# Optimization experiments

Hardware: AMD Instinct MI355X
Metric: run time of the kernel (lower is better)

## Reference

```python
import jax, jax.numpy as jnp
import numpy as np

B, T, C, H = 4, 2048, 1024, 16
HS = C // H  # head_size = 64
EPS = 1e-5


def setup_inputs() -> dict:
    key = jax.random.key(0)
    ks = jax.random.split(key, 16)
    s = 0.02
    inp = {
        "x": jax.random.normal(ks[0], (B, T, C), jnp.float32),
        # custom LayerNorm buffers (gamma=ones, beta=zeros in source)
        "ln1_g": jnp.ones((C,), jnp.float32),
        "ln1_b": jnp.zeros((C,), jnp.float32),
        "ln2_g": jnp.ones((C,), jnp.float32),
        "ln2_b": jnp.zeros((C,), jnp.float32),
        # per-head Q/K/V linears, stacked over heads: [H, C, HS]
        "Wq": jax.random.normal(ks[1], (H, C, HS), jnp.float32) * s,
        "bq": jax.random.normal(ks[2], (H, HS), jnp.float32) * s,
        "Wk": jax.random.normal(ks[3], (H, C, HS), jnp.float32) * s,
        "bk": jax.random.normal(ks[4], (H, HS), jnp.float32) * s,
        "Wv": jax.random.normal(ks[5], (H, C, HS), jnp.float32) * s,
        "bv": jax.random.normal(ks[6], (H, HS), jnp.float32) * s,
        # output projection [C, C]
        "Wo": jax.random.normal(ks[7], (C, C), jnp.float32) * s,
        "bo": jax.random.normal(ks[8], (C,), jnp.float32) * s,
        # FFN: C -> 4C -> C
        "W1": jax.random.normal(ks[9], (C, 4 * C), jnp.float32) * s,
        "b1": jax.random.normal(ks[10], (4 * C,), jnp.float32) * s,
        "W2": jax.random.normal(ks[11], (4 * C, C), jnp.float32) * s,
        "b2": jax.random.normal(ks[12], (C,), jnp.float32) * s,
    }
    return inp


def _layernorm_time_axis(x, g, b):
    # Faithful to source: normalizes over axis=1 (time), unbiased variance (ddof=1).
    m = jnp.mean(x, axis=1, keepdims=True)
    v = jnp.var(x, axis=1, keepdims=True, ddof=1)
    return g * (x - m) / jnp.sqrt(v + EPS) + b


def reference(x, ln1_g, ln1_b, ln2_g, ln2_b, Wq, bq, Wk, bk, Wv, bv, Wo, bo, W1, b1, W2, b2):
    Bc, Tc, Cc = x.shape
    h = _layernorm_time_axis(x, ln1_g, ln1_b)
    # per-head projections: [B, H, T, HS]
    q = jnp.einsum('btc,hcd->bhtd', h, Wq) + bq[None, :, None, :]
    k = jnp.einsum('btc,hcd->bhtd', h, Wk) + bk[None, :, None, :]
    v = jnp.einsum('btc,hcd->bhtd', h, Wv) + bv[None, :, None, :]
    # scores scaled by C**-0.5 (full embed dim, as in source)
    wei = jnp.einsum('bhtd,bhsd->bhts', q, k) * (Cc ** -0.5)
    causal = jnp.tril(jnp.ones((Tc, Tc), bool))
    wei = jnp.where(causal[None, None], wei, -jnp.inf)
    wei = jax.nn.softmax(wei, axis=-1)
    att = jnp.einsum('bhts,bhsd->bhtd', wei, v)
    # concat heads -> [B, T, C], then projection
    att = att.transpose(0, 2, 1, 3).reshape(Bc, Tc, Cc)
    x = x + att @ Wo + bo
    # FFN on ln2
    h2 = _layernorm_time_axis(x, ln2_g, ln2_b)
    ff = jax.nn.relu(h2 @ W1 + b1) @ W2 + b2
    return x + ff
```

## Files before the change

### kernel.cpp

```cpp
#include <hip/hip_runtime.h>

#define B_   4
#define T_   2048
#define C_   1024
#define H_   16
#define HS_  64
#define BT_  (B_*T_)
#define EPS_ 1e-5f

typedef unsigned short u16;
typedef unsigned int   u32;
typedef __attribute__((ext_vector_type(8))) __bf16 bf16x8;
typedef __attribute__((ext_vector_type(4))) float  f32x4;
typedef __attribute__((ext_vector_type(8))) u16    u16x8;
typedef __attribute__((ext_vector_type(4))) u16    u16x4;
typedef __attribute__((ext_vector_type(4))) u32    u32x4;

__device__ __forceinline__ u16 f2bf(float f) {
  unsigned x = __builtin_bit_cast(unsigned, f);
  x += 0x7fffu + ((x >> 16) & 1u);
  return (u16)(x >> 16);
}
__device__ __forceinline__ float bf2f(u16 v) {
  return __builtin_bit_cast(float, (u32)v << 16);
}

__device__ __forceinline__ float fast_exp2(float x) {
  float y;
  asm("v_exp_f32 %0, %1" : "=v"(y) : "v"(x));
  return y;
}
__device__ __forceinline__ float fast_rcp(float x) {
  float y;
  asm("v_rcp_f32 %0, %1" : "=v"(y) : "v"(x));
  return y;
}

#define GLD_LDS16(src, dst) \
  __builtin_amdgcn_global_load_lds((__attribute__((address_space(1))) void*)(src), \
                                   (__attribute__((address_space(3))) void*)(dst), 16, 0, 0)

__global__ __launch_bounds__(256) void ln_partial(const float* __restrict__ x,
                                                  float* __restrict__ ps,
                                                  float* __restrict__ psq) {
  int col = blockIdx.x * 256 + threadIdx.x;
  int b = col >> 10, c = col & (C_ - 1);
  int t0 = blockIdx.y * (T_ / 16);
  const float* p = x + (size_t)b * T_ * C_ + (size_t)t0 * C_ + c;
  float s = 0.f, sq = 0.f;
  #pragma unroll 4
  for (int i = 0; i < T_ / 16; ++i) { float v = p[(size_t)i * C_]; s += v; sq += v * v; }
  ps [blockIdx.y * (B_ * C_) + col] = s;
  psq[blockIdx.y * (B_ * C_) + col] = sq;
}

__global__ __launch_bounds__(256) void ln_partial_bf(const u16* __restrict__ x,
                                                     float* __restrict__ ps,
                                                     float* __restrict__ psq) {
  int col = blockIdx.x * 256 + threadIdx.x;
  int b = col >> 10, c = col & (C_ - 1);
  int t0 = blockIdx.y * (T_ / 16);
  const u16* p = x + (size_t)b * T_ * C_ + (size_t)t0 * C_ + c;
  float s = 0.f, sq = 0.f;
  #pragma unroll 4
  for (int i = 0; i < T_ / 16; ++i) { float v = bf2f(p[(size_t)i * C_]); s += v; sq += v * v; }
  ps [blockIdx.y * (B_ * C_) + col] = s;
  psq[blockIdx.y * (B_ * C_) + col] = sq;
}

__global__ __launch_bounds__(256) void ln_final(const float* __restrict__ ps,
                                                const float* __restrict__ psq,
                                                float* __restrict__ mean,
                                                float* __restrict__ rstd) {
  int col = blockIdx.x * 256 + threadIdx.x;
  float s = 0.f, sq = 0.f;
  #pragma unroll
  for (int i = 0; i < 16; ++i) { s += ps[i * (B_ * C_) + col]; sq += psq[i * (B_ * C_) + col]; }
  float m = s * (1.f / T_);
  float var = (sq - (float)T_ * m * m) * (1.f / (T_ - 1));
  mean[col] = m;
  rstd[col] = rsqrtf(var + EPS_);
}

__global__ __launch_bounds__(256) void ln_norm(const float* __restrict__ x,
                                               const float* __restrict__ mean,
                                               const float* __restrict__ rstd,
                                               const float* __restrict__ gam,
                                               const float* __restrict__ bet,
                                               u16* __restrict__ out) {
  size_t i = ((size_t)blockIdx.x * 256 + threadIdx.x) * 4;
  int c  = (int)(i & (C_ - 1));
  int b  = (int)(i >> 21);
  int bc = (b << 10) + c;
  float4 v = *(const float4*)(x + i);
  float vv[4] = {v.x, v.y, v.z, v.w};
  u16x4 o;
  #pragma unroll
  for (int j = 0; j < 4; ++j)
    o[j] = f2bf(gam[c + j] * (vv[j] - mean[bc + j]) * rstd[bc + j] + bet[c + j]);
  *(u16x4*)(out + i) = o;
}

__global__ __launch_bounds__(256) void ln_norm_bf(const u16* __restrict__ x,
                                                  const float* __restrict__ mean,
                                                  const float* __restrict__ rstd,
                                                  const float* __restrict__ gam,
                                                  const float* __restrict__ bet,
                                                  u16* __restrict__ out) {
  size_t i = ((size_t)blockIdx.x * 256 + threadIdx.x) * 4;
  int c  = (int)(i & (C_ - 1));
  int b  = (int)(i >> 21);
  int bc = (b << 10) + c;
  u16x4 v = *(const u16x4*)(x + i);
  u16x4 o;
  #pragma unroll
  for (int j = 0; j < 4; ++j)
    o[j] = f2bf(gam[c + j] * (bf2f(v[j]) - mean[bc + j]) * rstd[bc + j] + bet[c + j]);
  *(u16x4*)(out + i) = o;
}

__global__ __launch_bounds__(256) void transpose_cast(const float* __restrict__ in,
                                                      u16* __restrict__ out,
                                                      int cols_in, int ld_out,
                                                      size_t batch_in, size_t batch_out) {
  __shared__ float tile[32][33];
  const float* I = in + (size_t)blockIdx.z * batch_in;
  u16* Ou = out + (size_t)blockIdx.z * batch_out;
  int r0 = blockIdx.y << 5, c0 = blockIdx.x << 5;
  int tx = threadIdx.x & 31, ty = threadIdx.x >> 5;
  #pragma unroll
  for (int rr = 0; rr < 32; rr += 8)
    tile[ty + rr][tx] = I[(size_t)(r0 + ty + rr) * cols_in + c0 + tx];
  __syncthreads();
  #pragma unroll
  for (int rr = 0; rr < 32; rr += 8)
    Ou[(size_t)(c0 + ty + rr) * ld_out + r0 + tx] = f2bf(tile[tx][ty + rr]);
}

__global__ __launch_bounds__(256) void concat_bias(const float* __restrict__ bq,
                                                   const float* __restrict__ bk,
                                                   const float* __restrict__ bv,
                                                   float* __restrict__ out) {
  int i = blockIdx.x * 256 + threadIdx.x;
  float v = (i < 1024) ? bq[i] : (i < 2048 ? bk[i - 1024] : bv[i - 2048]);
  out[i] = v;
}

__global__ __launch_bounds__(256) void v_transpose(const u16* __restrict__ qkv,
                                                   u16* __restrict__ Vt) {
  __shared__ u16 tile[32][33];
  int bh = blockIdx.z; int b = bh >> 4, h = bh & 15;
  int t0 = blockIdx.x << 5, hs0 = blockIdx.y << 5;
  int tx = threadIdx.x & 31, ty = threadIdx.x >> 5;
  const u16* src = qkv + (size_t)(b * T_ + t0) * 3072 + 2048 + h * 64 + hs0;
  #pragma unroll
  for (int rr = 0; rr < 32; rr += 8)
    tile[ty + rr][tx] = src[(size_t)(ty + rr) * 3072 + tx];
  __syncthreads();
  u16* dst = Vt + ((size_t)bh * 64 + hs0) * T_ + t0;
  #pragma unroll
  for (int rr = 0; rr < 32; rr += 8)
    dst[(size_t)(ty + rr) * T_ + tx] = tile[tx][ty + rr];
}

template<int BN, int RELU, int QSCALE>
__global__ __launch_bounds__(256, 2)
void gemm_128t(const u16* __restrict__ A,
               const u16* __restrict__ Bt,
               const float* __restrict__ bias,
               u16* __restrict__ outp,
               int M, int N, int K) {
  constexpr int BK  = 32;
  constexpr int CHA = 2;
  constexpr int CHB = BN / 64;
  constexpr int NF  = BN / 32;

  __shared__ u16 sA[3][128 * BK];
  __shared__ u16 sB[3][BN * BK];

  const int tid = threadIdx.x;
  const int wave = tid >> 6, lane = tid & 63;
  const int g = lane >> 4, r16 = lane & 15;

  const int nbx = N / BN;
  const int nwg = gridDim.x;
  const int bid = blockIdx.x;
  const int swz = ((bid & 7) * (nwg >> 3)) + (bid >> 3);
  const int bx = swz % nbx, by = swz / nbx;
  const int row0 = by << 7, col0 = bx * BN;

  const u16* aS[CHA];
  const u16* bS[CHB];
  #pragma unroll
  for (int j = 0; j < CHA; ++j) {
    const int ci = tid + 256 * j, row = ci >> 2, cc = ci & 3;
    aS[j] = A + (size_t)(row0 + row) * K + ((cc ^ ((row >> 1) & 3)) * 8);
  }
  #pragma unroll
  for (int j = 0; j < CHB; ++j) {
    const int ci = tid + 256 * j, row = ci >> 2, cc = ci & 3;
    bS[j] = Bt + (size_t)(col0 + row) * K + ((cc ^ ((row >> 1) & 3)) * 8);
  }
  const int ldsOff = wave * 512;

  auto stage = [&](int t, int buf) {
    const int ko = t * BK;
    #pragma unroll
    for (int j = 0; j < CHA; ++j)
      GLD_LDS16(aS[j] + ko, &sA[buf][ldsOff + j * 2048]);
    #pragma unroll
    for (int j = 0; j < CHB; ++j)
      GLD_LDS16(bS[j] + ko, &sB[buf][ldsOff + j * 2048]);
  };

  auto wait_stage1 = [&]() {
    if constexpr (CHB == 4) asm volatile("s_waitcnt vmcnt(6)" ::: "memory");
    else                    asm volatile("s_waitcnt vmcnt(5)" ::: "memory");
  };

  const int wrow = (wave >> 1) * 64;
  const int wcol = (wave & 1) * (BN >> 1);
  f32x4 acc[4][NF] = {};

  const int NT = K / BK;

  stage(0, 0); stage(1, 1);
  wait_stage1();
  __builtin_amdgcn_s_barrier();
  __builtin_amdgcn_sched_barrier(0);

  for (int t = 0; t < NT; ++t) {
    const u16* As = sA[t % 3];
    const u16* Bs = sB[t % 3];
    bf16x8 af[4], bf[NF];
    #pragma unroll
    for (int m = 0; m < 4; ++m) {
      const int lr = wrow + m * 16 + r16;
      af[m] = *(const bf16x8*)&As[lr * 32 + ((g ^ ((lr >> 1) & 3)) * 8)];
    }
    #pragma unroll
    for (int n = 0; n < NF; ++n) {
      const int lr = wcol + n * 16 + r16;
      bf[n] = *(const bf16x8*)&Bs[lr * 32 + ((g ^ ((lr >> 1) & 3)) * 8)];
    }
    if (t + 2 < NT) stage(t + 2, (t + 2) % 3);

    __builtin_amdgcn_s_setprio(1);
    #pragma unroll
    for (int m = 0; m < 4; ++m)
      #pragma unroll
      for (int n = 0; n < NF; ++n)
        acc[m][n] = __builtin_amdgcn_mfma_f32_16x16x32_bf16(af[m], bf[n], acc[m][n], 0, 0, 0);
    __builtin_amdgcn_s_setprio(0);

    if (t + 1 < NT) {
      if (t + 2 < NT) wait_stage1();
      else            asm volatile("s_waitcnt vmcnt(0)" ::: "memory");
      __builtin_amdgcn_s_barrier();
      __builtin_amdgcn_sched_barrier(0);
    }
  }

  #pragma unroll
  for (int m = 0; m < 4; ++m) {
    #pragma unroll
    for (int n = 0; n < NF; ++n) {
      const int col = col0 + wcol + n * 16 + r16;
      const float bv = bias[col];
      const float sc = (QSCALE && col < 1024) ? 0.04508422003f : 1.f;
      const int rowb = row0 + wrow + m * 16 + g * 4;
      #pragma unroll
      for (int r = 0; r < 4; ++r) {
        float v = acc[m][n][r] + bv;
        if (RELU) v = fmaxf(v, 0.f);
        if (QSCALE) v *= sc;
        outp[(size_t)(rowb + r) * N + col] = f2bf(v);
      }
    }
  }
}

template<int RELU, int RAW, int QSCALE>
__global__ __launch_bounds__(512, 2)
void gemm_256(const u16* __restrict__ A,
              const u16* __restrict__ Bt,
              const float* __restrict__ bias,
              const u16* __restrict__ resb,
              void* __restrict__ outp,
              void* __restrict__ outp_b,
              int M, int N, int K) {
  constexpr int BK = 32;
  __shared__ u16 sA[4][256 * BK];
  __shared__ u16 sB[4][256 * BK];

  const int tid = threadIdx.x;
  const int wave = tid >> 6, lane = tid & 63;
  const int g = lane >> 4, r16 = lane & 15;

  const int nbx = N >> 8;
  const int nwg = gridDim.x;
  const int bid = blockIdx.x;
  const int swz = ((bid & 7) * (nwg >> 3)) + (bid >> 3);
  const int bx = swz % nbx, by = swz / nbx;
  const int row0 = by << 8, col0 = bx << 8;

  const int kspan = RAW ? (K >> 1) : K;
  const int kbase = RAW ? ((int)blockIdx.y * kspan) : 0;

  const u16* aS[2];
  const u16* bS[2];
  #pragma unroll
  for (int j = 0; j < 2; ++j) {
    const int ci = tid + 512 * j, row = ci >> 2, cc = ci & 3;
    aS[j] = A  + (size_t)(row0 + row) * K + ((cc ^ ((row >> 1) & 3)) * 8) + kbase;
    bS[j] = Bt + (size_t)(col0 + row) * K + ((cc ^ ((row >> 1) & 3)) * 8) + kbase;
  }
  const int ldsOff = wave * 512;

  auto stage = [&](int t, int buf) {
    const int ko = t * BK;
    #pragma unroll
    for (int j = 0; j < 2; ++j)
      GLD_LDS16(aS[j] + ko, &sA[buf][ldsOff + j * 4096]);
    #pragma unroll
    for (int j = 0; j < 2; ++j)
      GLD_LDS16(bS[j] + ko, &sB[buf][ldsOff + j * 4096]);
  };

  const int wrow = (wave >> 2) * 128;
  const int wcol = (wave & 3) * 64;
  f32x4 acc[8][4] = {};

  const int NT = kspan / BK;

  stage(0, 0); stage(1, 1);
  asm volatile("s_waitcnt vmcnt(4)" ::: "memory");
  __builtin_amdgcn_s_barrier();
  __builtin_amdgcn_sched_barrier(0);

  for (int t = 0; t < NT; ++t) {
    const u16* As = sA[t & 3];
    const u16* Bs = sB[t & 3];
    bf16x8 af[8], bf[4];
    #pragma unroll
    for (int m = 0; m < 8; ++m) {
      const int lr = wrow + m * 16 + r16;
      af[m] = *(const bf16x8*)&As[lr * 32 + ((g ^ ((lr >> 1) & 3)) * 8)];
    }
    #pragma unroll
    for (int n = 0; n < 4; ++n) {
      const int lr = wcol + n * 16 + r16;
      bf[n] = *(const bf16x8*)&Bs[lr * 32 + ((g ^ ((lr >> 1) & 3)) * 8)];
    }
    if (t + 2 < NT) stage(t + 2, (t + 2) & 3);

    __builtin_amdgcn_s_setprio(1);
    #pragma unroll
    for (int m = 0; m < 8; ++m)
      #pragma unroll
      for (int n = 0; n < 4; ++n)
        acc[m][n] = __builtin_amdgcn_mfma_f32_16x16x32_bf16(af[m], bf[n], acc[m][n], 0, 0, 0);
    __builtin_amdgcn_s_setprio(0);

    if (t + 1 < NT) {
      if (t + 2 < NT) asm volatile("s_waitcnt vmcnt(4)" ::: "memory");
      else            asm volatile("s_waitcnt vmcnt(0)" ::: "memory");
      __builtin_amdgcn_s_barrier();
      __builtin_amdgcn_sched_barrier(0);
    }
  }

  if constexpr (RAW) {
    if (blockIdx.y) {
      float* po = (float*)outp_b;
      #pragma unroll
      for (int m = 0; m < 8; ++m) {
        #pragma unroll
        for (int n = 0; n < 4; ++n) {
          const int col = col0 + wcol + n * 16 + r16;
          const float bv = bias[col];
          const int rowb = row0 + wrow + m * 16 + g * 4;
          #pragma unroll
          for (int r = 0; r < 4; ++r) {
            const size_t idx = (size_t)(rowb + r) * N + col;
            po[idx] = acc[m][n][r] + bv + bf2f(resb[idx]);
          }
        }
      }
    } else {
      float* po = (float*)outp;
      #pragma unroll
      for (int m = 0; m < 8; ++m) {
        #pragma unroll
        for (int n = 0; n < 4; ++n) {
          const int col = col0 + wcol + n * 16 + r16;
          const int rowb = row0 + wrow + m * 16 + g * 4;
          #pragma unroll
          for (int r = 0; r < 4; ++r)
            po[(size_t)(rowb + r) * N + col] = acc[m][n][r];
        }
      }
    }
  } else {
    u16* po = (u16*)outp;
    #pragma unroll
    for (int m = 0; m < 8; ++m) {
      #pragma unroll
      for (int n = 0; n < 4; ++n) {
        const int col = col0 + wcol + n * 16 + r16;
        const float bv = bias[col];
        const float sc = (QSCALE && col < 1024) ? 0.04508422003f : 1.f;
        const int rowb = row0 + wrow + m * 16 + g * 4;
        #pragma unroll
        for (int r = 0; r < 4; ++r) {
          float v = acc[m][n][r] + bv;
          if (RELU) v = fmaxf(v, 0.f);
          if (QSCALE) v *= sc;
          po[(size_t)(rowb + r) * N + col] = f2bf(v);
        }
      }
    }
  }
}

__global__ __launch_bounds__(256) void ffn2_reduce(const float* __restrict__ pA,
                                                   float* __restrict__ out) {
  size_t i = ((size_t)blockIdx.x * 256 + threadIdx.x) * 4;
  float4 a = *(const float4*)(pA + i);
  float4 o = *(const float4*)(out + i);
  float4 v;
  v.x = a.x + o.x;
  v.y = a.y + o.y;
  v.z = a.z + o.z;
  v.w = a.w + o.w;
  *(float4*)(out + i) = v;
}

template<int BM, int BN, int THREADS, int OUT_F32, int RELU, int RES>
__global__ __launch_bounds__(THREADS, 3)
void gemm_pipe(const u16* __restrict__ A,
               const u16* __restrict__ Bt,
               const float* __restrict__ bias,
               const float* __restrict__ res,
               void* __restrict__ outp,
               int M, int N, int K) {
  constexpr int BK  = 32;
  constexpr int CHA = (BM * 4) / THREADS;
  constexpr int CHB = (BN * 4) / THREADS;
  constexpr int CH  = CHA + CHB;

  __shared__ u16 sA[3][BM * BK];
  __shared__ u16 sB[3][BN * BK];

  const int tid = threadIdx.x;
  const int wave = tid >> 6, lane = tid & 63;
  const int g = lane >> 4, r16 = lane & 15;

  const int nbx = N / BN;
  const int nwg = gridDim.x;
  const int bid = blockIdx.x;
  const int swz = ((bid & 7) * (nwg >> 3)) + (bid >> 3);
  const int bx = swz % nbx, by = swz / nbx;
  const int row0 = by * BM, col0 = bx * BN;

  const u16* aS[CHA];
  const u16* bS[CHB];
  #pragma unroll
  for (int j = 0; j < CHA; ++j) {
    const int ci = tid + THREADS * j, row = ci >> 2, cc = ci & 3;
    aS[j] = A + (size_t)(row0 + row) * K + ((cc ^ ((row >> 1) & 3)) * 8);
  }
  #pragma unroll
  for (int j = 0; j < CHB; ++j) {
    const int ci = tid + THREADS * j, row = ci >> 2, cc = ci & 3;
    bS[j] = Bt + (size_t)(col0 + row) * K + ((cc ^ ((row >> 1) & 3)) * 8);
  }
  const int ldsOff = wave * 512;

  auto stage = [&](int t, int buf) {
    const int ko = t * BK;
    #pragma unroll
    for (int j = 0; j < CHA; ++j)
      GLD_LDS16(aS[j] + ko, &sA[buf][ldsOff + j * (THREADS * 8)]);
    #pragma unroll
    for (int j = 0; j < CHB; ++j)
      GLD_LDS16(bS[j] + ko, &sB[buf][ldsOff + j * (THREADS * 8)]);
  };

  const int wrow = (wave >> 1) * 64;
  const int wcol = (wave & 1) * 64;
  f32x4 acc[4][4] = {};

  const int NT = K / BK;

  stage(0, 0); stage(1, 1);
  if constexpr (CH == 3) asm volatile("s_waitcnt vmcnt(3)" ::: "memory");
  else                   asm volatile("s_waitcnt vmcnt(4)" ::: "memory");
  __builtin_amdgcn_s_barrier();
  __builtin_amdgcn_sched_barrier(0);

  for (int t = 0; t < NT; ++t) {
    if (t + 2 < NT) stage(t + 2, (t + 2) % 3);
    const u16* As = sA[t % 3];
    const u16* Bs = sB[t % 3];
    bf16x8 af[4], bf[4];
    #pragma unroll
    for (int m = 0; m < 4; ++m) {
      const int lr = wrow + m * 16 + r16;
      af[m] = *(const bf16x8*)&As[lr * 32 + ((g ^ ((lr >> 1) & 3)) * 8)];
    }
    #pragma unroll
    for (int n = 0; n < 4; ++n) {
      const int lr = wcol + n * 16 + r16;
      bf[n] = *(const bf16x8*)&Bs[lr * 32 + ((g ^ ((lr >> 1) & 3)) * 8)];
    }
    __builtin_amdgcn_s_setprio(1);
    #pragma unroll
    for (int m = 0; m < 4; ++m)
      #pragma unroll
      for (int n = 0; n < 4; ++n)
        acc[m][n] = __builtin_amdgcn_mfma_f32_16x16x32_bf16(af[m], bf[n], acc[m][n], 0, 0, 0);
    __builtin_amdgcn_s_setprio(0);

    if (t + 1 < NT) {
      if (t + 2 < NT) {
        if constexpr (CH == 3) asm volatile("s_waitcnt vmcnt(3)" ::: "memory");
        else                   asm volatile("s_waitcnt vmcnt(4)" ::: "memory");
      } else {
        asm volatile("s_waitcnt vmcnt(0)" ::: "memory");
      }
      __builtin_amdgcn_s_barrier();
      __builtin_amdgcn_sched_barrier(0);
    }
  }

  #pragma unroll
  for (int m = 0; m < 4; ++m) {
    #pragma unroll
    for (int n = 0; n < 4; ++n) {
      const int col = col0 + wcol + n * 16 + r16;
      const float bv = bias[col];
      const int rowb = row0 + wrow + m * 16 + g * 4;
      #pragma unroll
      for (int r = 0; r < 4; ++r) {
        const size_t idx = (size_t)(rowb + r) * N + col;
        float v = acc[m][n][r] + bv;
        if (RES)  v += res[idx];
        if (RELU) v = fmaxf(v, 0.f);
        if (OUT_F32) ((float*)outp)[idx] = v;
        else         ((u16*)outp)[idx]   = f2bf(v);
      }
    }
  }
}

__global__ __launch_bounds__(256, 4) void attn_fwd(const u16* __restrict__ qkv,
                                                   const u16* __restrict__ Vt,
                                                   u16* __restrict__ O) {
  __shared__ u16 sK[2][64 * 64];
  __shared__ u16 sV[2][64 * 64];

  const int orig = blockIdx.x;
  const int work = ((orig & 7) << 7) + (orig >> 3);
  const int i = work & 15;
  const int h = (work >> 4) & 15;
  const int b = work >> 8;
  const int qA = i << 6, qB = (31 - i) << 6;
  const int nA = i + 1,  nB = 32 - i;

  const int tid = threadIdx.x, wave = tid >> 6, lane = tid & 63;
  const int g = lane >> 4, r16 = lane & 15;

  const size_t base = (size_t)b * T_ * 3072 + h * 64;
  const u16* Qp = qkv + base;
  const u16* Kp = qkv + base + 1024;
  const u16* VtP = Vt + (size_t)(b * 16 + h) * 64 * T_;

  const int rowL = lane >> 3;
  const int colL = 8 * ((lane & 7) ^ rowL);
  const u16* kSrc = Kp  + (size_t)(wave * 16 + rowL) * 3072 + colL;
  const u16* vSrc = VtP + (size_t)(wave * 16 + rowL) * T_   + colL;
  u16* kDst0 = &sK[0][(wave * 16 + 0) * 64];
  u16* kDst8 = &sK[0][(wave * 16 + 8) * 64];
  u16* vDst0 = &sV[0][(wave * 16 + 0) * 64];
  u16* vDst8 = &sV[0][(wave * 16 + 8) * 64];

  const int ck0 = (( 0 + g * 16) ^ ((r16 & 7) << 4)) >> 1;
  const int ck1 = ((64 + g * 16) ^ ((r16 & 7) << 4)) >> 1;

  bf16x8 qfA[2], qfB[2];
  #pragma unroll
  for (int kc = 0; kc < 2; ++kc) {
    qfA[kc] = *(const bf16x8*)(Qp + (size_t)(qA + wave * 16 + r16) * 3072 + kc * 32 + g * 8);
    qfB[kc] = *(const bf16x8*)(Qp + (size_t)(qB + wave * 16 + r16) * 3072 + kc * 32 + g * 8);
  }

  f32x4 accA[4] = {}, accB[4] = {};
  f32x4 lA4 = {}, lB4 = {};
  const int qaA = qA + wave * 16 + r16;
  const int qaB = qB + wave * 16 + r16;

  const u32 one2 = 0x3F803F80u;
  const u32x4 onesv = {one2, one2, one2, one2};
  const bf16x8 ONES = __builtin_bit_cast(bf16x8, onesv);

  int sbuf = 0;
  auto stageAdv = [&]() {
    const int o = sbuf * 4096;
    GLD_LDS16(kSrc,            kDst0 + o);
    GLD_LDS16(kSrc + 8 * 3072, kDst8 + o);
    GLD_LDS16(vSrc,            vDst0 + o);
    GLD_LDS16(vSrc + 8 * T_,   vDst8 + o);
    kSrc += 64 * 3072;
    vSrc += 64;
    sbuf ^= 1;
  };

  auto qkt = [&](const bf16x8* kf0, const bf16x8* kf1, const bf16x8* qf, f32x4* s) {
    __builtin_amdgcn_s_setprio(1);
    #pragma unroll
    for (int ni = 0; ni < 4; ++ni) {
      f32x4 t = {};
      t = __builtin_amdgcn_mfma_f32_16x16x32_bf16(kf0[ni], qf[0], t, 0, 0, 0);
      t = __builtin_amdgcn_mfma_f32_16x16x32_bf16(kf1[ni], qf[1], t, 0, 0, 0);
      s[ni] = t;
    }
    __builtin_amdgcn_s_setprio(0);
  };

  auto softmax_pack = [&](f32x4* s, bool diag, int q_abs, int kv0, bf16x8* pa) {
    if (diag) {
      #pragma unroll
      for (int ni = 0; ni < 4; ++ni)
        #pragma unroll
        for (int r = 0; r < 4; ++r) {
          const int kv_abs = kv0 + ni * 16 + g * 4 + r;
          if (kv_abs > q_abs) s[ni][r] = -3e38f;
        }
    }
    #pragma unroll
    for (int ni = 0; ni < 4; ++ni)
      #pragma unroll
      for (int r = 0; r < 4; ++r)
        s[ni][r] = fast_exp2(s[ni][r]);

    u32 pk[4][2];
    #pragma unroll
    for (int ni = 0; ni < 4; ++ni)
      #pragma unroll
      for (int h2 = 0; h2 < 2; ++h2)
        asm("v_cvt_pk_bf16_f32 %0, %1, %2"
            : "=v"(pk[ni][h2]) : "v"(s[ni][2 * h2]), "v"(s[ni][2 * h2 + 1]));

    u32 pa32[2][4];
    #pragma unroll
    for (int kc = 0; kc < 2; ++kc)
      #pragma unroll
      for (int h2 = 0; h2 < 2; ++h2) {
        u32 a = pk[2 * kc][h2], bq_ = pk[2 * kc + 1][h2];
        asm("v_permlane32_swap_b32 %0, %1" : "+v"(a), "+v"(bq_));
        asm("v_permlane16_swap_b32 %0, %1" : "+v"(a), "+v"(bq_));
        pa32[kc][h2] = a;
        pa32[kc][2 + h2] = bq_;
      }
    #pragma unroll
    for (int kc = 0; kc < 2; ++kc) {
      u32x4 tmp = {pa32[kc][0], pa32[kc][1], pa32[kc][2], pa32[kc][3]};
      pa[kc] = __builtin_bit_cast(bf16x8, tmp);
    }
  };

  stageAdv();
  asm volatile("s_waitcnt vmcnt(0)" ::: "memory");
  __builtin_amdgcn_s_barrier();
  __builtin_amdgcn_sched_barrier(0);

  int cbuf = 0;
  for (int t = 0; t < nB; ++t) {
    if (t + 1 < nB) stageAdv();
    const u16* Kb = sK[cbuf];
    const u16* Vb = sV[cbuf];
    const int kv0 = t << 6;
    const bool actA = (t < nA);

    bf16x8 kf0[4], kf1[4];
    #pragma unroll
    for (int ni = 0; ni < 4; ++ni) {
      kf0[ni] = *(const bf16x8*)&Kb[(ni * 16 + r16) * 64 + ck0];
      kf1[ni] = *(const bf16x8*)&Kb[(ni * 16 + r16) * 64 + ck1];
    }

    f32x4 s[4];
    bf16x8 paB[2], paA[2];

    qkt(kf0, kf1, qfB, s);
    softmax_pack(s, t == nB - 1, qaB, kv0, paB);
    if (actA) {
      qkt(kf0, kf1, qfA, s);
      softmax_pack(s, t == nA - 1, qaA, kv0, paA);
    }

    bf16x8 vf0[4], vf1[4];
    #pragma unroll
    for (int hsb = 0; hsb < 4; ++hsb) {
      vf0[hsb] = *(const bf16x8*)&Vb[(hsb * 16 + r16) * 64 + ck0];
      vf1[hsb] = *(const bf16x8*)&Vb[(hsb * 16 + r16) * 64 + ck1];
    }

    __builtin_amdgcn_s_setprio(1);
    lB4 = __builtin_amdgcn_mfma_f32_16x16x32_bf16(paB[0], ONES, lB4, 0, 0, 0);
    lB4 = __builtin_amdgcn_mfma_f32_16x16x32_bf16(paB[1], ONES, lB4, 0, 0, 0);
    #pragma unroll
    for (int hsb = 0; hsb < 4; ++hsb) {
      accB[hsb] = __builtin_amdgcn_mfma_f32_16x16x32_bf16(paB[0], vf0[hsb], accB[hsb], 0, 0, 0);
      accB[hsb] = __builtin_amdgcn_mfma_f32_16x16x32_bf16(paB[1], vf1[hsb], accB[hsb], 0, 0, 0);
    }
    if (actA) {
      lA4 = __builtin_amdgcn_mfma_f32_16x16x32_bf16(paA[0], ONES, lA4, 0, 0, 0);
      lA4 = __builtin_amdgcn_mfma_f32_16x16x32_bf16(paA[1], ONES, lA4, 0, 0, 0);
      #pragma unroll
      for (int hsb = 0; hsb < 4; ++hsb) {
        accA[hsb] = __builtin_amdgcn_mfma_f32_16x16x32_bf16(paA[0], vf0[hsb], accA[hsb], 0, 0, 0);
        accA[hsb] = __builtin_amdgcn_mfma_f32_16x16x32_bf16(paA[1], vf1[hsb], accA[hsb], 0, 0, 0);
      }
    }
    __builtin_amdgcn_s_setprio(0);

    if (t + 1 < nB) {
      asm volatile("s_waitcnt vmcnt(0)" ::: "memory");
      __builtin_amdgcn_s_barrier();
      __builtin_amdgcn_sched_barrier(0);
    }
    cbuf ^= 1;
  }

  float rlA[4], rlB[4];
  #pragma unroll
  for (int r = 0; r < 4; ++r) {
    rlA[r] = fast_rcp(lA4[r]);
    rlB[r] = fast_rcp(lB4[r]);
  }
  #pragma unroll
  for (int hsb = 0; hsb < 4; ++hsb)
    #pragma unroll
    for (int r = 0; r < 4; ++r) {
      const size_t rowA = (size_t)b * T_ + qA + wave * 16 + g * 4 + r;
      const size_t rowB = (size_t)b * T_ + qB + wave * 16 + g * 4 + r;
      O[rowA * C_ + h * 64 + hsb * 16 + r16] = f2bf(accA[hsb][r] * rlA[r]);
      O[rowB * C_ + h * 64 + hsb * 16 + r16] = f2bf(accB[hsb][r] * rlB[r]);
    }
}

extern "C" void kernel_launch(void* const* d_in, const int* in_sizes, int n_in,
                              void* d_out, int out_size, void* d_ws, size_t ws_size,
                              hipStream_t stream) {
  const float* x    = (const float*)d_in[0];
  const float* ln1g = (const float*)d_in[1];
  const float* ln1b = (const float*)d_in[2];
  const float* ln2g = (const float*)d_in[3];
  const float* ln2b = (const float*)d_in[4];
  const float* Wq   = (const float*)d_in[5];
  const float* bq   = (const float*)d_in[6];
  const float* Wk   = (const float*)d_in[7];
  const float* bk   = (const float*)d_in[8];
  const float* Wv   = (const float*)d_in[9];
  const float* bv   = (const float*)d_in[10];
  const float* Wo   = (const float*)d_in[11];
  const float* bo   = (const float*)d_in[12];
  const float* W1   = (const float*)d_in[13];
  const float* b1   = (const float*)d_in[14];
  const float* W2   = (const float*)d_in[15];
  const float* b2   = (const float*)d_in[16];

  char* w = (char*)d_ws;
  float* ps    = (float*)(w + 0);
  float* psq   = (float*)(w + 262144);
  float* mean  = (float*)(w + 524288);
  float* rstd  = (float*)(w + 540672);
  float* bqkv  = (float*)(w + 557056);
  u16*   h     = (u16*)  (w + 573440);
  u16*   wqkvT = (u16*)  (w + 17350656);
  u16*   woT   = (u16*)  (w + 23642112);
  u16*   w1T   = (u16*)  (w + 25739264);
  u16*   w2T   = (u16*)  (w + 34127872);
  u16*   x1b   = (u16*)  (w + 42516480);
  u16*   Vt    = (u16*)  (w + 59293696);
  u16*   qkv   = (u16*)  (w + 76070912);
  u16*   Oo    = (u16*)  (w + 126402560);
  u16*   u     = qkv;
  float* pA    = (float*)(w + 573440);

  transpose_cast<<<dim3(2, 32, 16), 256, 0, stream>>>(Wq, wqkvT,                     64,   1024, (size_t)C_ * 64, (size_t)64 * 1024);
  transpose_cast<<<dim3(2, 32, 16), 256, 0, stream>>>(Wk, wqkvT + (size_t)1024*1024, 64,   1024, (size_t)C_ * 64, (size_t)64 * 1024);
  transpose_cast<<<dim3(2, 32, 16), 256, 0, stream>>>(Wv, wqkvT + (size_t)2048*1024, 64,   1024, (size_t)C_ * 64, (size_t)64 * 1024);
  transpose_cast<<<dim3(32, 32, 1), 256, 0, stream>>>(Wo, woT, 1024, 1024, 0, 0);
  transpose_cast<<<dim3(128, 32, 1), 256, 0, stream>>>(W1, w1T, 4096, 1024, 0, 0);
  transpose_cast<<<dim3(32, 128, 1), 256, 0, stream>>>(W2, w2T, 1024, 4096, 0, 0);
  concat_bias<<<12, 256, 0, stream>>>(bq, bk, bv, bqkv);

  ln_partial<<<dim3(16, 16), 256, 0, stream>>>(x, ps, psq);
  ln_final<<<16, 256, 0, stream>>>(ps, psq, mean, rstd);
  ln_norm<<<8192, 256, 0, stream>>>(x, mean, rstd, ln1g, ln1b, h);

  gemm_128t<192, 0, 1><<<1024, 256, 0, stream>>>(h, wqkvT, bqkv, qkv, BT_, 3072, 1024);

  v_transpose<<<dim3(T_ / 32, 2, B_ * H_), 256, 0, stream>>>(qkv, Vt);

  attn_fwd<<<1024, 256, 0, stream>>>(qkv, Vt, Oo);

  gemm_pipe<128, 128, 256, 0, 0, 1><<<512, 256, 0, stream>>>(Oo, woT, bo, x, x1b, BT_, 1024, 1024);

  ln_partial_bf<<<dim3(16, 16), 256, 0, stream>>>(x1b, ps, psq);
  ln_final<<<16, 256, 0, stream>>>(ps, psq, mean, rstd);
  ln_norm_bf<<<8192, 256, 0, stream>>>(x1b, mean, rstd, ln2g, ln2b, h);

  gemm_128t<256, 1, 0><<<1024, 256, 0, stream>>>(h, w1T, b1, u, BT_, 4096, 1024);
  gemm_256<0, 1, 0><<<dim3(128, 2), 512, 0, stream>>>(u, w2T, b2, x1b, pA, d_out, BT_, 1024, 4096);
  ffn2_reduce<<<8192, 256, 0, stream>>>(pA, (float*)d_out);
}
```

Baseline: 393.4 us.

## Process 128-row query tiles per attention block to double K/V reuse

```diff
diff --git a/kernel.cpp b/kernel.cpp
--- a/kernel.cpp
+++ b/kernel.cpp
@@ -554,19 +554,19 @@
   }
 }
 
-__global__ __launch_bounds__(256, 4) void attn_fwd(const u16* __restrict__ qkv,
+__global__ __launch_bounds__(256, 2) void attn_fwd(const u16* __restrict__ qkv,
                                                    const u16* __restrict__ Vt,
                                                    u16* __restrict__ O) {
   __shared__ u16 sK[2][64 * 64];
   __shared__ u16 sV[2][64 * 64];
 
   const int orig = blockIdx.x;
-  const int work = ((orig & 7) << 7) + (orig >> 3);
-  const int i = work & 15;
-  const int h = (work >> 4) & 15;
-  const int b = work >> 8;
-  const int qA = i << 6, qB = (31 - i) << 6;
-  const int nA = i + 1,  nB = 32 - i;
+  const int work = ((orig & 7) << 6) + (orig >> 3);
+  const int i = work & 7;
+  const int h = (work >> 3) & 15;
+  const int b = work >> 7;
+  const int qA = i << 7, qB = (15 - i) << 7;
+  const int nA = 2 * i + 2, nB = 32 - 2 * i;
 
   const int tid = threadIdx.x, wave = tid >> 6, lane = tid & 63;
   const int g = lane >> 4, r16 = lane & 15;
@@ -588,17 +588,23 @@
   const int ck0 = (( 0 + g * 16) ^ ((r16 & 7) << 4)) >> 1;
   const int ck1 = ((64 + g * 16) ^ ((r16 & 7) << 4)) >> 1;
 
-  bf16x8 qfA[2], qfB[2];
-  #pragma unroll
-  for (int kc = 0; kc < 2; ++kc) {
-    qfA[kc] = *(const bf16x8*)(Qp + (size_t)(qA + wave * 16 + r16) * 3072 + kc * 32 + g * 8);
-    qfB[kc] = *(const bf16x8*)(Qp + (size_t)(qB + wave * 16 + r16) * 3072 + kc * 32 + g * 8);
-  }
-
-  f32x4 accA[4] = {}, accB[4] = {};
-  f32x4 lA4 = {}, lB4 = {};
-  const int qaA = qA + wave * 16 + r16;
-  const int qaB = qB + wave * 16 + r16;
+  bf16x8 qfA[2][2], qfB[2][2];
+  #pragma unroll
+  for (int qp = 0; qp < 2; ++qp)
+    #pragma unroll
+    for (int kc = 0; kc < 2; ++kc) {
+      qfA[qp][kc] = *(const bf16x8*)(Qp + (size_t)(qA + wave * 32 + qp * 16 + r16) * 3072 + kc * 32 + g * 8);
+      qfB[qp][kc] = *(const bf16x8*)(Qp + (size_t)(qB + wave * 32 + qp * 16 + r16) * 3072 + kc * 32 + g * 8);
+    }
+
+  f32x4 accA[2][4] = {}, accB[2][4] = {};
+  f32x4 lA[2] = {}, lB[2] = {};
+  int qaA[2], qaB[2];
+  #pragma unroll
+  for (int qp = 0; qp < 2; ++qp) {
+    qaA[qp] = qA + wave * 32 + qp * 16 + r16;
+    qaB[qp] = qB + wave * 32 + qp * 16 + r16;
+  }
 
   const u32 one2 = 0x3F803F80u;
   const u32x4 onesv = {one2, one2, one2, one2};
@@ -682,49 +688,53 @@
     const u16* Vb = sV[cbuf];
     const int kv0 = t << 6;
     const bool actA = (t < nA);
-
-    bf16x8 kf0[4], kf1[4];
+    const bool mB = (t + 2 >= nB);
+    const bool mA = (t + 2 >= nA);
+
+    bf16x8 kf0[4], kf1[4], vf0[4], vf1[4];
     #pragma unroll
     for (int ni = 0; ni < 4; ++ni) {
       kf0[ni] = *(const bf16x8*)&Kb[(ni * 16 + r16) * 64 + ck0];
       kf1[ni] = *(const bf16x8*)&Kb[(ni * 16 + r16) * 64 + ck1];
-    }
-
-    f32x4 s[4];
-    bf16x8 paB[2], paA[2];
-
-    qkt(kf0, kf1, qfB, s);
-    softmax_pack(s, t == nB - 1, qaB, kv0, paB);
+      vf0[ni] = *(const bf16x8*)&Vb[(ni * 16 + r16) * 64 + ck0];
+      vf1[ni] = *(const bf16x8*)&Vb[(ni * 16 + r16) * 64 + ck1];
+    }
+
+    #pragma unroll
+    for (int qp = 0; qp < 2; ++qp) {
+      f32x4 s[4];
+      bf16x8 pa[2];
+      qkt(kf0, kf1, qfB[qp], s);
+      softmax_pack(s, mB, qaB[qp], kv0, pa);
+      __builtin_amdgcn_s_setprio(1);
+      lB[qp] = __builtin_amdgcn_mfma_f32_16x16x32_bf16(pa[0], ONES, lB[qp], 0, 0, 0);
+      lB[qp] = __builtin_amdgcn_mfma_f32_16x16x32_bf16(pa[1], ONES, lB[qp], 0, 0, 0);
+      #pragma unroll
+      for (int hsb = 0; hsb < 4; ++hsb) {
+        accB[qp][hsb] = __builtin_amdgcn_mfma_f32_16x16x32_bf16(pa[0], vf0[hsb], accB[qp][hsb], 0, 0, 0);
+        accB[qp][hsb] = __builtin_amdgcn_mfma_f32_16x16x32_bf16(pa[1], vf1[hsb], accB[qp][hsb], 0, 0, 0);
+      }
+      __builtin_amdgcn_s_setprio(0);
+    }
+
     if (actA) {
-      qkt(kf0, kf1, qfA, s);
-      softmax_pack(s, t == nA - 1, qaA, kv0, paA);
-    }
-
-    bf16x8 vf0[4], vf1[4];
-    #pragma unroll
-    for (int hsb = 0; hsb < 4; ++hsb) {
-      vf0[hsb] = *(const bf16x8*)&Vb[(hsb * 16 + r16) * 64 + ck0];
-      vf1[hsb] = *(const bf16x8*)&Vb[(hsb * 16 + r16) * 64 + ck1];
-    }
-
-    __builtin_amdgcn_s_setprio(1);
-    lB4 = __builtin_amdgcn_mfma_f32_16x16x32_bf16(paB[0], ONES, lB4, 0, 0, 0);
-    lB4 = __builtin_amdgcn_mfma_f32_16x16x32_bf16(paB[1], ONES, lB4, 0, 0, 0);
-    #pragma unroll
-    for (int hsb = 0; hsb < 4; ++hsb) {
-      accB[hsb] = __builtin_amdgcn_mfma_f32_16x16x32_bf16(paB[0], vf0[hsb], accB[hsb], 0, 0, 0);
-      accB[hsb] = __builtin_amdgcn_mfma_f32_16x16x32_bf16(paB[1], vf1[hsb], accB[hsb], 0, 0, 0);
-    }
-    if (actA) {
-      lA4 = __builtin_amdgcn_mfma_f32_16x16x32_bf16(paA[0], ONES, lA4, 0, 0, 0);
-      lA4 = __builtin_amdgcn_mfma_f32_16x16x32_bf16(paA[1], ONES, lA4, 0, 0, 0);
-      #pragma unroll
-      for (int hsb = 0; hsb < 4; ++hsb) {
-        accA[hsb] = __builtin_amdgcn_mfma_f32_16x16x32_bf16(paA[0], vf0[hsb], accA[hsb], 0, 0, 0);
-        accA[hsb] = __builtin_amdgcn_mfma_f32_16x16x32_bf16(paA[1], vf1[hsb], accA[hsb], 0, 0, 0);
-      }
-    }
-    __builtin_amdgcn_s_setprio(0);
+      #pragma unroll
+      for (int qp = 0; qp < 2; ++qp) {
+        f32x4 s[4];
+        bf16x8 pa[2];
+        qkt(kf0, kf1, qfA[qp], s);
+        softmax_pack(s, mA, qaA[qp], kv0, pa);
+        __builtin_amdgcn_s_setprio(1);
+        lA[qp] = __builtin_amdgcn_mfma_f32_16x16x32_bf16(pa[0], ONES, lA[qp], 0, 0, 0);
+        lA[qp] = __builtin_amdgcn_mfma_f32_16x16x32_bf16(pa[1], ONES, lA[qp], 0, 0, 0);
+        #pragma unroll
+        for (int hsb = 0; hsb < 4; ++hsb) {
+          accA[qp][hsb] = __builtin_amdgcn_mfma_f32_16x16x32_bf16(pa[0], vf0[hsb], accA[qp][hsb], 0, 0, 0);
+          accA[qp][hsb] = __builtin_amdgcn_mfma_f32_16x16x32_bf16(pa[1], vf1[hsb], accA[qp][hsb], 0, 0, 0);
+        }
+        __builtin_amdgcn_s_setprio(0);
+      }
+    }
 
     if (t + 1 < nB) {
       asm volatile("s_waitcnt vmcnt(0)" ::: "memory");
@@ -734,21 +744,24 @@
     cbuf ^= 1;
   }
 
-  float rlA[4], rlB[4];
-  #pragma unroll
-  for (int r = 0; r < 4; ++r) {
-    rlA[r] = fast_rcp(lA4[r]);
-    rlB[r] = fast_rcp(lB4[r]);
-  }
-  #pragma unroll
-  for (int hsb = 0; hsb < 4; ++hsb)
+  #pragma unroll
+  for (int qp = 0; qp < 2; ++qp) {
+    float rlA[4], rlB[4];
     #pragma unroll
     for (int r = 0; r < 4; ++r) {
-      const size_t rowA = (size_t)b * T_ + qA + wave * 16 + g * 4 + r;
-      const size_t rowB = (size_t)b * T_ + qB + wave * 16 + g * 4 + r;
-      O[rowA * C_ + h * 64 + hsb * 16 + r16] = f2bf(accA[hsb][r] * rlA[r]);
-      O[rowB * C_ + h * 64 + hsb * 16 + r16] = f2bf(accB[hsb][r] * rlB[r]);
-    }
+      rlA[r] = fast_rcp(lA[qp][r]);
+      rlB[r] = fast_rcp(lB[qp][r]);
+    }
+    #pragma unroll
+    for (int hsb = 0; hsb < 4; ++hsb)
+      #pragma unroll
+      for (int r = 0; r < 4; ++r) {
+        const size_t rowA = (size_t)b * T_ + qA + wave * 32 + qp * 16 + g * 4 + r;
+        const size_t rowB = (size_t)b * T_ + qB + wave * 32 + qp * 16 + g * 4 + r;
+        O[rowA * C_ + h * 64 + hsb * 16 + r16] = f2bf(accA[qp][hsb][r] * rlA[r]);
+        O[rowB * C_ + h * 64 + hsb * 16 + r16] = f2bf(accB[qp][hsb][r] * rlB[r]);
+      }
+  }
 }
 
 extern "C" void kernel_launch(void* const* d_in, const int* in_sizes, int n_in,
@@ -806,7 +819,7 @@
 
   v_transpose<<<dim3(T_ / 32, 2, B_ * H_), 256, 0, stream>>>(qkv, Vt);
 
-  attn_fwd<<<1024, 256, 0, stream>>>(qkv, Vt, Oo);
+  attn_fwd<<<512, 256, 0, stream>>>(qkv, Vt, Oo);
 
   gemm_pipe<128, 128, 256, 0, 0, 1><<<512, 256, 0, stream>>>(Oo, woT, bo, x, x1b, BT_, 1024, 1024);
 
```

New measurement: 382.1 us. 1.03x faster.
